# Kernel optimization log

Hardware: AMD Instinct MI355X
Metric: run time of the kernel (lower is better)

## Reference

```python
import jax, jax.numpy as jnp
import numpy as np

N, T, H, E = 16384, 4, 64, 262144
NEG_SLOPE = 0.2  # LeakyReLU slope for GAT-style attention
LN_EPS = 1e-5


def setup_inputs() -> dict:
    key = jax.random.key(0)
    ks = jax.random.split(key, 24)
    p = {}
    p["pred"] = jax.random.normal(ks[0], (N, T, H), jnp.float32)
    p["ei_structural"] = jax.random.randint(ks[1], (2, E), 0, N, jnp.int32)
    p["ei_functional"] = jax.random.randint(ks[2], (2, E), 0, N, jnp.int32)
    scale = 1.0 / np.sqrt(H)
    i = 3
    for l in range(2):
        for et in ("s", "f"):
            p[f"W{l}{et}"] = (jax.random.normal(ks[i], (H, H), jnp.float32) * scale); i += 1
            p[f"a{l}{et}"] = (jax.random.normal(ks[i], (H,), jnp.float32) * scale); i += 1
        p[f"g{l}"] = jnp.ones((H,), jnp.float32)
        p[f"b{l}"] = jnp.zeros((H,), jnp.float32)
    return p


def _conv(x, ei, W, a, n_dst):
    """Attention-based ST graph conv, temporal_kernel_size=1 (per-step)."""
    h = jnp.einsum('nth,hd->ntd', x, W)          # [N,T,H] linear transform
    src, dst = ei[0], ei[1]
    he = h[src]                                   # [E,T,H] gather per edge
    logits = jax.nn.leaky_relu(jnp.einsum('eth,h->et', he, a), NEG_SLOPE)
    m = jax.ops.segment_max(logits, dst, num_segments=n_dst)     # [N,T]
    ex = jnp.exp(logits - m[dst])                 # stable softmax over incoming edges
    den = jax.ops.segment_sum(ex, dst, num_segments=n_dst)
    alpha = ex / den[dst]                         # [E,T]
    return jax.ops.segment_sum(alpha[..., None] * he, dst, num_segments=n_dst)


def _ln(x, g, b):
    mu = x.mean(-1, keepdims=True)
    v = x.var(-1, keepdims=True)
    return (x - mu) * jax.lax.rsqrt(v + LN_EPS) * g + b


def reference(pred, ei_structural, ei_functional,
              W0s, a0s, W0f, a0f, g0, b0,
              W1s, a1s, W1f, a1f, g1, b1):
    x = pred
    layers = ((W0s, a0s, W0f, a0f, g0, b0), (W1s, a1s, W1f, a1f, g1, b1))
    for (Ws, av, Wf, af, g, b) in layers:
        ms = _conv(x, ei_structural, Ws, av, N)
        mf = _conv(x, ei_functional, Wf, af, N)
        # sum(messages)/len(messages), residual, LayerNorm over H (dropout=identity in eval)
        x = _ln(x + 0.5 * (ms + mf), g, b)
    return x
```

## Files before the change

kernel.cpp:

```cpp
#include <hip/hip_runtime.h>
#include <hip/hip_bf16.h>

#define NN 16384
#define TT 4
#define HH 64
#define NT (NN * TT)
#define CAP 128
#define NEG_SLOPE 0.2f
#define LN_EPS 1e-5f

typedef __attribute__((ext_vector_type(8))) short short8;
typedef __attribute__((ext_vector_type(4))) float f32x4;

__device__ __forceinline__ float bf2f(unsigned short u) {
    return __uint_as_float((unsigned)u << 16);
}
__device__ __forceinline__ unsigned short f2bf(float f) {
    unsigned u = __float_as_uint(f);
    return (unsigned short)((u + 0x7FFF + ((u >> 16) & 1)) >> 16);
}


__global__ void zero_kernel(int* __restrict__ a, int n) {
    int i = blockIdx.x * blockDim.x + threadIdx.x;
    if (i < n) a[i] = 0;
}

__global__ void scatter_bucket_kernel(const int* __restrict__ ei_s, const int* __restrict__ ei_f,
                                      int* __restrict__ cnt2, int* __restrict__ col2, int E) {
    int e = blockIdx.x * blockDim.x + threadIdx.x;
    if (e < E) {
        int d = ei_s[E + e];
        int pos = atomicAdd(&cnt2[d], 1);
        if (pos < CAP) col2[d * CAP + pos] = ei_s[e];
    } else {
        e -= E;
        if (e < E) {
            int d = ei_f[E + e];
            int pos = atomicAdd(&cnt2[NN + d], 1);
            if (pos < CAP) col2[(long)NN * CAP + d * CAP + pos] = ei_f[e];
        }
    }
}


__global__ __launch_bounds__(256) void transform2_kernel(
    const float4* __restrict__ x4,
    const float* __restrict__ Ws, const float* __restrict__ as_,
    const float* __restrict__ Wf, const float* __restrict__ af,
    unsigned short* __restrict__ h_s, float* __restrict__ esc_s,
    unsigned short* __restrict__ h_f, float* __restrict__ esc_f) {
    const int lane = threadIdx.x & 63;
    const int wv = threadIdx.x >> 6;
    const int m = lane & 15;
    const int quad = lane >> 4;

    short8 Bs[4][2], Bf[4][2];
#pragma unroll
    for (int c = 0; c < 4; c++) {
#pragma unroll
        for (int ks = 0; ks < 2; ks++) {
#pragma unroll
            for (int j = 0; j < 8; j++) {
                int k = ks * 32 + quad * 8 + j;
                int n = c * 16 + m;
                Bs[c][ks][j] = (short)f2bf(Ws[k * 64 + n]);
                Bf[c][ks][j] = (short)f2bf(Wf[k * 64 + n]);
            }
        }
    }
    float a_s[4], a_f[4];
#pragma unroll
    for (int c = 0; c < 4; c++) { a_s[c] = as_[c * 16 + m]; a_f[c] = af[c * 16 + m]; }

    const int rowbase = blockIdx.x * 128 + wv * 32;
#pragma unroll
    for (int rt = 0; rt < 2; rt++) {
        const int row0 = rowbase + rt * 16;
        const long xbase = (long)(row0 + m) * 16 + quad * 2;
        float4 xa = x4[xbase];
        float4 xb = x4[xbase + 1];
        float4 xc = x4[xbase + 8];
        float4 xd = x4[xbase + 9];
        short8 A0, A1;
        A0[0] = (short)f2bf(xa.x); A0[1] = (short)f2bf(xa.y);
        A0[2] = (short)f2bf(xa.z); A0[3] = (short)f2bf(xa.w);
        A0[4] = (short)f2bf(xb.x); A0[5] = (short)f2bf(xb.y);
        A0[6] = (short)f2bf(xb.z); A0[7] = (short)f2bf(xb.w);
        A1[0] = (short)f2bf(xc.x); A1[1] = (short)f2bf(xc.y);
        A1[2] = (short)f2bf(xc.z); A1[3] = (short)f2bf(xc.w);
        A1[4] = (short)f2bf(xd.x); A1[5] = (short)f2bf(xd.y);
        A1[6] = (short)f2bf(xd.z); A1[7] = (short)f2bf(xd.w);

        f32x4 accs[4], accf[4];
#pragma unroll
        for (int c = 0; c < 4; c++) {
            accs[c] = (f32x4){0.f, 0.f, 0.f, 0.f};
            accf[c] = (f32x4){0.f, 0.f, 0.f, 0.f};
        }
#pragma unroll
        for (int c = 0; c < 4; c++) {
            accs[c] = __builtin_amdgcn_mfma_f32_16x16x32_bf16(A0, Bs[c][0], accs[c], 0, 0, 0);
            accs[c] = __builtin_amdgcn_mfma_f32_16x16x32_bf16(A1, Bs[c][1], accs[c], 0, 0, 0);
            accf[c] = __builtin_amdgcn_mfma_f32_16x16x32_bf16(A0, Bf[c][0], accf[c], 0, 0, 0);
            accf[c] = __builtin_amdgcn_mfma_f32_16x16x32_bf16(A1, Bf[c][1], accf[c], 0, 0, 0);
        }
#pragma unroll
        for (int reg = 0; reg < 4; reg++) {
            const int row = row0 + quad * 4 + reg;
            float ps = 0.f, pf = 0.f;
#pragma unroll
            for (int c = 0; c < 4; c++) {
                h_s[(long)row * 64 + c * 16 + m] = f2bf(accs[c][reg]);
                h_f[(long)row * 64 + c * 16 + m] = f2bf(accf[c][reg]);
                ps = fmaf(accs[c][reg], a_s[c], ps);
                pf = fmaf(accf[c][reg], a_f[c], pf);
            }
#pragma unroll
            for (int off = 1; off < 16; off <<= 1) {
                ps += __shfl_xor(ps, off, 64);
                pf += __shfl_xor(pf, off, 64);
            }
            if (m == 0) {
                float ls = (ps > 0.f) ? ps : NEG_SLOPE * ps;
                float lf = (pf > 0.f) ? pf : NEG_SLOPE * pf;
                esc_s[row] = __expf(ls);
                esc_f[row] = __expf(lf);
            }
        }
    }
}


__global__ __launch_bounds__(256) void aggregate_kernel(
    const float4* __restrict__ x4,
    const ushort4* __restrict__ hs4, const float* __restrict__ escs,
    const int* __restrict__ cnts, const int* __restrict__ cols,
    const ushort4* __restrict__ hf4, const float* __restrict__ escf,
    const int* __restrict__ cntf, const int* __restrict__ colf,
    const float4* __restrict__ g4, const float4* __restrict__ b4,
    float4* __restrict__ out4) {
    const int wv = threadIdx.x >> 6;
    const int lane = threadIdx.x & 63;
    const int n = blockIdx.x * 4 + wv;
    const int t = lane >> 4;
    const int ci = lane & 15;

    int cS = cnts[n]; if (cS > CAP) cS = CAP;
    int cF = cntf[n]; if (cF > CAP) cF = CAP;
    cS = __builtin_amdgcn_readfirstlane(cS);
    cF = __builtin_amdgcn_readfirstlane(cF);
    const int* colS = cols + (long)n * CAP;
    const int* colF = colf + (long)n * CAP;

    int idxS = colS[lane];
    int idxF = colF[lane];
    if (lane >= cS) idxS = 0;
    if (lane >= cF) idxF = 0;

    const int cS64 = cS < 64 ? cS : 64;
    const int cF64 = cF < 64 ? cF : 64;

    float dS = 0.f, sx = 0.f, sy = 0.f, sz = 0.f, sw = 0.f;
    float dF = 0.f, fx = 0.f, fy = 0.f, fz = 0.f, fw = 0.f;

    const int nbS = (cS64 + 7) >> 3;
    const int nbF = (cF64 + 7) >> 3;
    const int nb = nbS > nbF ? nbS : nbF;

    for (int it = 0; it < nb; ++it) {
        const int j = it << 3;
        const bool doS = it < nbS;
        const bool doF = it < nbF;
        int sS[8], sF[8];
        float eS[8], eF[8];
        ushort4 hS[8], hF[8];

        if (doS) {
#pragma unroll
            for (int u = 0; u < 8; u++) sS[u] = __builtin_amdgcn_readlane(idxS, j + u);
#pragma unroll
            for (int u = 0; u < 8; u++) hS[u] = hs4[sS[u] * 64 + lane];
#pragma unroll
            for (int u = 0; u < 8; u++) eS[u] = escs[sS[u] * 4 + t];
        }
        if (doF) {
#pragma unroll
            for (int u = 0; u < 8; u++) sF[u] = __builtin_amdgcn_readlane(idxF, j + u);
#pragma unroll
            for (int u = 0; u < 8; u++) hF[u] = hf4[sF[u] * 64 + lane];
#pragma unroll
            for (int u = 0; u < 8; u++) eF[u] = escf[sF[u] * 4 + t];
        }
        if (doS) {
#pragma unroll
            for (int u = 0; u < 8; u++) {
                float e = (j + u < cS64) ? eS[u] : 0.f;
                dS += e;
                sx = fmaf(e, bf2f(hS[u].x), sx);
                sy = fmaf(e, bf2f(hS[u].y), sy);
                sz = fmaf(e, bf2f(hS[u].z), sz);
                sw = fmaf(e, bf2f(hS[u].w), sw);
            }
        }
        if (doF) {
#pragma unroll
            for (int u = 0; u < 8; u++) {
                float e = (j + u < cF64) ? eF[u] : 0.f;
                dF += e;
                fx = fmaf(e, bf2f(hF[u].x), fx);
                fy = fmaf(e, bf2f(hF[u].y), fy);
                fz = fmaf(e, bf2f(hF[u].z), fz);
                fw = fmaf(e, bf2f(hF[u].w), fw);
            }
        }
    }

    for (int j2 = 64; j2 < cS; ++j2) {
        int s0 = colS[j2];
        float e0 = escs[s0 * 4 + t];
        ushort4 h0 = hs4[(long)s0 * 64 + lane];
        dS += e0;
        sx = fmaf(e0, bf2f(h0.x), sx);
        sy = fmaf(e0, bf2f(h0.y), sy);
        sz = fmaf(e0, bf2f(h0.z), sz);
        sw = fmaf(e0, bf2f(h0.w), sw);
    }
    for (int j2 = 64; j2 < cF; ++j2) {
        int s0 = colF[j2];
        float e0 = escf[s0 * 4 + t];
        ushort4 h0 = hf4[(long)s0 * 64 + lane];
        dF += e0;
        fx = fmaf(e0, bf2f(h0.x), fx);
        fy = fmaf(e0, bf2f(h0.y), fy);
        fz = fmaf(e0, bf2f(h0.z), fz);
        fw = fmaf(e0, bf2f(h0.w), fw);
    }

    float msx = 0.f, msy = 0.f, msz = 0.f, msw = 0.f;
    if (dS > 0.f) {
        float r = 1.f / dS;
        msx = sx * r; msy = sy * r; msz = sz * r; msw = sw * r;
    }
    float mfx = 0.f, mfy = 0.f, mfz = 0.f, mfw = 0.f;
    if (dF > 0.f) {
        float r = 1.f / dF;
        mfx = fx * r; mfy = fy * r; mfz = fz * r; mfw = fw * r;
    }

    float4 xv = x4[(long)n * 64 + lane];
    float v0 = xv.x + 0.5f * (msx + mfx);
    float v1 = xv.y + 0.5f * (msy + mfy);
    float v2 = xv.z + 0.5f * (msz + mfz);
    float v3 = xv.w + 0.5f * (msw + mfw);

    float sum = (v0 + v1) + (v2 + v3);
#pragma unroll
    for (int off = 1; off < 16; off <<= 1) sum += __shfl_xor(sum, off, 64);
    float mu = sum * (1.f / 64.f);
    float d0 = v0 - mu, d1 = v1 - mu, d2 = v2 - mu, d3 = v3 - mu;
    float var = (d0 * d0 + d1 * d1) + (d2 * d2 + d3 * d3);
#pragma unroll
    for (int off = 1; off < 16; off <<= 1) var += __shfl_xor(var, off, 64);
    var *= (1.f / 64.f);
    float inv = rsqrtf(var + LN_EPS);
    float4 gv = g4[ci], bv = b4[ci];
    float4 o;
    o.x = d0 * inv * gv.x + bv.x;
    o.y = d1 * inv * gv.y + bv.y;
    o.z = d2 * inv * gv.z + bv.z;
    o.w = d3 * inv * gv.w + bv.w;
    out4[(long)n * 64 + lane] = o;
}


extern "C" void kernel_launch(void* const* d_in, const int* in_sizes, int n_in,
                              void* d_out, int out_size, void* d_ws, size_t ws_size,
                              hipStream_t stream) {
    const float* pred = (const float*)d_in[0];
    const int* ei_s = (const int*)d_in[1];
    const int* ei_f = (const int*)d_in[2];
    const float* W0s = (const float*)d_in[3];
    const float* a0s = (const float*)d_in[4];
    const float* W0f = (const float*)d_in[5];
    const float* a0f = (const float*)d_in[6];
    const float* g0  = (const float*)d_in[7];
    const float* b0  = (const float*)d_in[8];
    const float* W1s = (const float*)d_in[9];
    const float* a1s = (const float*)d_in[10];
    const float* W1f = (const float*)d_in[11];
    const float* a1f = (const float*)d_in[12];
    const float* g1  = (const float*)d_in[13];
    const float* b1  = (const float*)d_in[14];
    const int E = in_sizes[1] / 2;

    char* ws = (char*)d_ws;
    auto alloc = [&](size_t bytes) {
        char* p = ws;
        ws += (bytes + 255) & ~(size_t)255;
        return p;
    };
    int* cnt2 = (int*)alloc((size_t)2 * NN * sizeof(int));
    int* col2 = (int*)alloc((size_t)2 * NN * CAP * sizeof(int));
    unsigned short* h_s = (unsigned short*)alloc((size_t)NT * HH * sizeof(unsigned short));
    unsigned short* h_f = (unsigned short*)alloc((size_t)NT * HH * sizeof(unsigned short));
    float* esc_s = (float*)alloc((size_t)NT * sizeof(float));
    float* esc_f = (float*)alloc((size_t)NT * sizeof(float));
    float* x_mid = (float*)alloc((size_t)NT * HH * sizeof(float));

    const int* cnt_s = cnt2;
    const int* cnt_f = cnt2 + NN;
    const int* col_s = col2;
    const int* col_f = col2 + (size_t)NN * CAP;

    const int EB = (E + 255) / 256;

    zero_kernel<<<(2 * NN) / 256, 256, 0, stream>>>(cnt2, 2 * NN);
    scatter_bucket_kernel<<<2 * EB, 256, 0, stream>>>(ei_s, ei_f, cnt2, col2, E);

    transform2_kernel<<<NT / 128, 256, 0, stream>>>(
        (const float4*)pred, W0s, a0s, W0f, a0f, h_s, esc_s, h_f, esc_f);
    aggregate_kernel<<<NN / 4, 256, 0, stream>>>(
        (const float4*)pred, (const ushort4*)h_s, esc_s, cnt_s, col_s,
        (const ushort4*)h_f, esc_f, cnt_f, col_f,
        (const float4*)g0, (const float4*)b0, (float4*)x_mid);

    transform2_kernel<<<NT / 128, 256, 0, stream>>>(
        (const float4*)x_mid, W1s, a1s, W1f, a1f, h_s, esc_s, h_f, esc_f);
    aggregate_kernel<<<NN / 4, 256, 0, stream>>>(
        (const float4*)x_mid, (const ushort4*)h_s, esc_s, cnt_s, col_s,
        (const ushort4*)h_f, esc_f, cnt_f, col_f,
        (const float4*)g1, (const float4*)b1, (float4*)d_out);
}
```

Measured before the change: 220.0 us.

## Fuse all stages into persistent mega-kernel with software grid barriers

```diff
diff --git a/kernel.cpp b/kernel.cpp
--- a/kernel.cpp
+++ b/kernel.cpp
@@ -8,6 +8,7 @@
 #define CAP 128
 #define NEG_SLOPE 0.2f
 #define LN_EPS 1e-5f
+#define MEGA_BLOCKS 512
 
 typedef __attribute__((ext_vector_type(8))) short short8;
 typedef __attribute__((ext_vector_type(4))) float f32x4;
@@ -21,21 +22,66 @@
 }
 
 
-__global__ void zero_kernel(int* __restrict__ a, int n) {
-    int i = blockIdx.x * blockDim.x + threadIdx.x;
-    if (i < n) a[i] = 0;
-}
-
-__global__ void scatter_bucket_kernel(const int* __restrict__ ei_s, const int* __restrict__ ei_f,
-                                      int* __restrict__ cnt2, int* __restrict__ col2, int E) {
-    int e = blockIdx.x * blockDim.x + threadIdx.x;
-    if (e < E) {
-        int d = ei_s[E + e];
-        int pos = atomicAdd(&cnt2[d], 1);
-        if (pos < CAP) col2[d * CAP + pos] = ei_s[e];
-    } else {
-        e -= E;
+__device__ __forceinline__ void gridbar(int* bar) {
+    __syncthreads();
+    if (threadIdx.x == 0) {
+        __threadfence();
+        int g = __hip_atomic_load(&bar[1], __ATOMIC_RELAXED, __HIP_MEMORY_SCOPE_AGENT);
+        int a = atomicAdd(&bar[0], 1);
+        if (a == MEGA_BLOCKS - 1) {
+            __hip_atomic_store(&bar[0], 0, __ATOMIC_RELAXED, __HIP_MEMORY_SCOPE_AGENT);
+            __hip_atomic_store(&bar[1], g + 1, __ATOMIC_RELEASE, __HIP_MEMORY_SCOPE_AGENT);
+        } else {
+            while (__hip_atomic_load(&bar[1], __ATOMIC_ACQUIRE, __HIP_MEMORY_SCOPE_AGENT) == g)
+                __builtin_amdgcn_s_sleep(2);
+        }
+        __threadfence();
+    }
+    __syncthreads();
+}
+
+
+__global__ __launch_bounds__(256) void prep_kernel(
+    const float* __restrict__ W0s_, const float* __restrict__ W0f_,
+    const float* __restrict__ W1s_, const float* __restrict__ W1f_,
+    short8* __restrict__ wpack, int* __restrict__ cnt2, int* __restrict__ bar) {
+    const int b = blockIdx.x;
+    if (b < 128) {
+        cnt2[b * 256 + threadIdx.x] = 0;
+        if (b == 0 && threadIdx.x < 2) bar[threadIdx.x] = 0;
+        return;
+    }
+    int id = (b - 128) * 256 + threadIdx.x;
+    int mat = id >> 9;
+    int slot = id & 511;
+    int lane = slot & 63;
+    int cks = slot >> 6;
+    int c = cks >> 1, ks = cks & 1;
+    int m = lane & 15, quad = lane >> 4;
+    const float* W = (mat == 0) ? W0s_ : (mat == 1) ? W0f_ : (mat == 2) ? W1s_ : W1f_;
+    short8 v;
+#pragma unroll
+    for (int j = 0; j < 8; j++) {
+        int k = ks * 32 + quad * 8 + j;
+        int n = c * 16 + m;
+        v[j] = (short)f2bf(W[k * 64 + n]);
+    }
+    wpack[id] = v;
+}
+
+
+__device__ __forceinline__ void scatter_body(const int* __restrict__ ei_s,
+                                             const int* __restrict__ ei_f,
+                                             int* __restrict__ cnt2,
+                                             int* __restrict__ col2, int E) {
+    for (int e0 = blockIdx.x * 256 + threadIdx.x; e0 < 2 * E; e0 += MEGA_BLOCKS * 256) {
+        int e = e0;
         if (e < E) {
+            int d = ei_s[E + e];
+            int pos = atomicAdd(&cnt2[d], 1);
+            if (pos < CAP) col2[d * CAP + pos] = ei_s[e];
+        } else {
+            e -= E;
             int d = ei_f[E + e];
             int pos = atomicAdd(&cnt2[NN + d], 1);
             if (pos < CAP) col2[(long)NN * CAP + d * CAP + pos] = ei_f[e];
@@ -44,10 +90,10 @@
 }
 
 
-__global__ __launch_bounds__(256) void transform2_kernel(
+__device__ __forceinline__ void transform_body(
     const float4* __restrict__ x4,
-    const float* __restrict__ Ws, const float* __restrict__ as_,
-    const float* __restrict__ Wf, const float* __restrict__ af,
+    const short8* __restrict__ wp_s, const float* __restrict__ as_,
+    const short8* __restrict__ wp_f, const float* __restrict__ af,
     unsigned short* __restrict__ h_s, float* __restrict__ esc_s,
     unsigned short* __restrict__ h_f, float* __restrict__ esc_f) {
     const int lane = threadIdx.x & 63;
@@ -60,13 +106,8 @@
     for (int c = 0; c < 4; c++) {
 #pragma unroll
         for (int ks = 0; ks < 2; ks++) {
-#pragma unroll
-            for (int j = 0; j < 8; j++) {
-                int k = ks * 32 + quad * 8 + j;
-                int n = c * 16 + m;
-                Bs[c][ks][j] = (short)f2bf(Ws[k * 64 + n]);
-                Bf[c][ks][j] = (short)f2bf(Wf[k * 64 + n]);
-            }
+            Bs[c][ks] = wp_s[(c * 2 + ks) * 64 + lane];
+            Bf[c][ks] = wp_f[(c * 2 + ks) * 64 + lane];
         }
     }
     float a_s[4], a_f[4];
@@ -132,7 +173,7 @@
 }
 
 
-__global__ __launch_bounds__(256) void aggregate_kernel(
+__device__ __forceinline__ void aggregate_body(
     const float4* __restrict__ x4,
     const ushort4* __restrict__ hs4, const float* __restrict__ escs,
     const int* __restrict__ cnts, const int* __restrict__ cols,
@@ -142,135 +183,172 @@
     float4* __restrict__ out4) {
     const int wv = threadIdx.x >> 6;
     const int lane = threadIdx.x & 63;
-    const int n = blockIdx.x * 4 + wv;
     const int t = lane >> 4;
     const int ci = lane & 15;
-
-    int cS = cnts[n]; if (cS > CAP) cS = CAP;
-    int cF = cntf[n]; if (cF > CAP) cF = CAP;
-    cS = __builtin_amdgcn_readfirstlane(cS);
-    cF = __builtin_amdgcn_readfirstlane(cF);
-    const int* colS = cols + (long)n * CAP;
-    const int* colF = colf + (long)n * CAP;
-
-    int idxS = colS[lane];
-    int idxF = colF[lane];
-    if (lane >= cS) idxS = 0;
-    if (lane >= cF) idxF = 0;
-
-    const int cS64 = cS < 64 ? cS : 64;
-    const int cF64 = cF < 64 ? cF : 64;
-
-    float dS = 0.f, sx = 0.f, sy = 0.f, sz = 0.f, sw = 0.f;
-    float dF = 0.f, fx = 0.f, fy = 0.f, fz = 0.f, fw = 0.f;
-
-    const int nbS = (cS64 + 7) >> 3;
-    const int nbF = (cF64 + 7) >> 3;
-    const int nb = nbS > nbF ? nbS : nbF;
-
-    for (int it = 0; it < nb; ++it) {
-        const int j = it << 3;
-        const bool doS = it < nbS;
-        const bool doF = it < nbF;
-        int sS[8], sF[8];
-        float eS[8], eF[8];
-        ushort4 hS[8], hF[8];
-
-        if (doS) {
-#pragma unroll
-            for (int u = 0; u < 8; u++) sS[u] = __builtin_amdgcn_readlane(idxS, j + u);
-#pragma unroll
-            for (int u = 0; u < 8; u++) hS[u] = hs4[sS[u] * 64 + lane];
-#pragma unroll
-            for (int u = 0; u < 8; u++) eS[u] = escs[sS[u] * 4 + t];
-        }
-        if (doF) {
-#pragma unroll
-            for (int u = 0; u < 8; u++) sF[u] = __builtin_amdgcn_readlane(idxF, j + u);
-#pragma unroll
-            for (int u = 0; u < 8; u++) hF[u] = hf4[sF[u] * 64 + lane];
-#pragma unroll
-            for (int u = 0; u < 8; u++) eF[u] = escf[sF[u] * 4 + t];
-        }
-        if (doS) {
-#pragma unroll
-            for (int u = 0; u < 8; u++) {
-                float e = (j + u < cS64) ? eS[u] : 0.f;
-                dS += e;
-                sx = fmaf(e, bf2f(hS[u].x), sx);
-                sy = fmaf(e, bf2f(hS[u].y), sy);
-                sz = fmaf(e, bf2f(hS[u].z), sz);
-                sw = fmaf(e, bf2f(hS[u].w), sw);
-            }
-        }
-        if (doF) {
-#pragma unroll
-            for (int u = 0; u < 8; u++) {
-                float e = (j + u < cF64) ? eF[u] : 0.f;
-                dF += e;
-                fx = fmaf(e, bf2f(hF[u].x), fx);
-                fy = fmaf(e, bf2f(hF[u].y), fy);
-                fz = fmaf(e, bf2f(hF[u].z), fz);
-                fw = fmaf(e, bf2f(hF[u].w), fw);
-            }
-        }
-    }
-
-    for (int j2 = 64; j2 < cS; ++j2) {
-        int s0 = colS[j2];
-        float e0 = escs[s0 * 4 + t];
-        ushort4 h0 = hs4[(long)s0 * 64 + lane];
-        dS += e0;
-        sx = fmaf(e0, bf2f(h0.x), sx);
-        sy = fmaf(e0, bf2f(h0.y), sy);
-        sz = fmaf(e0, bf2f(h0.z), sz);
-        sw = fmaf(e0, bf2f(h0.w), sw);
-    }
-    for (int j2 = 64; j2 < cF; ++j2) {
-        int s0 = colF[j2];
-        float e0 = escf[s0 * 4 + t];
-        ushort4 h0 = hf4[(long)s0 * 64 + lane];
-        dF += e0;
-        fx = fmaf(e0, bf2f(h0.x), fx);
-        fy = fmaf(e0, bf2f(h0.y), fy);
-        fz = fmaf(e0, bf2f(h0.z), fz);
-        fw = fmaf(e0, bf2f(h0.w), fw);
-    }
-
-    float msx = 0.f, msy = 0.f, msz = 0.f, msw = 0.f;
-    if (dS > 0.f) {
-        float r = 1.f / dS;
-        msx = sx * r; msy = sy * r; msz = sz * r; msw = sw * r;
-    }
-    float mfx = 0.f, mfy = 0.f, mfz = 0.f, mfw = 0.f;
-    if (dF > 0.f) {
-        float r = 1.f / dF;
-        mfx = fx * r; mfy = fy * r; mfz = fz * r; mfw = fw * r;
-    }
-
-    float4 xv = x4[(long)n * 64 + lane];
-    float v0 = xv.x + 0.5f * (msx + mfx);
-    float v1 = xv.y + 0.5f * (msy + mfy);
-    float v2 = xv.z + 0.5f * (msz + mfz);
-    float v3 = xv.w + 0.5f * (msw + mfw);
-
-    float sum = (v0 + v1) + (v2 + v3);
-#pragma unroll
-    for (int off = 1; off < 16; off <<= 1) sum += __shfl_xor(sum, off, 64);
-    float mu = sum * (1.f / 64.f);
-    float d0 = v0 - mu, d1 = v1 - mu, d2 = v2 - mu, d3 = v3 - mu;
-    float var = (d0 * d0 + d1 * d1) + (d2 * d2 + d3 * d3);
-#pragma unroll
-    for (int off = 1; off < 16; off <<= 1) var += __shfl_xor(var, off, 64);
-    var *= (1.f / 64.f);
-    float inv = rsqrtf(var + LN_EPS);
-    float4 gv = g4[ci], bv = b4[ci];
-    float4 o;
-    o.x = d0 * inv * gv.x + bv.x;
-    o.y = d1 * inv * gv.y + bv.y;
-    o.z = d2 * inv * gv.z + bv.z;
-    o.w = d3 * inv * gv.w + bv.w;
-    out4[(long)n * 64 + lane] = o;
+    const float4 gv = g4[ci], bv = b4[ci];
+    const int n0 = (blockIdx.x * 4 + wv) * 8;
+
+    for (int i = 0; i < 8; ++i) {
+        const int n = n0 + i;
+        int cS = cnts[n]; if (cS > CAP) cS = CAP;
+        int cF = cntf[n]; if (cF > CAP) cF = CAP;
+        cS = __builtin_amdgcn_readfirstlane(cS);
+        cF = __builtin_amdgcn_readfirstlane(cF);
+        const int* colS = cols + (long)n * CAP;
+        const int* colF = colf + (long)n * CAP;
+
+        int idxS = colS[lane];
+        int idxF = colF[lane];
+        if (lane >= cS) idxS = 0;
+        if (lane >= cF) idxF = 0;
+
+        const int cS64 = cS < 64 ? cS : 64;
+        const int cF64 = cF < 64 ? cF : 64;
+
+        float dS = 0.f, sx = 0.f, sy = 0.f, sz = 0.f, sw = 0.f;
+        float dF = 0.f, fx = 0.f, fy = 0.f, fz = 0.f, fw = 0.f;
+
+        const int nbS = (cS64 + 7) >> 3;
+        const int nbF = (cF64 + 7) >> 3;
+        const int nb = nbS > nbF ? nbS : nbF;
+
+        for (int it = 0; it < nb; ++it) {
+            const int j = it << 3;
+            const bool doS = it < nbS;
+            const bool doF = it < nbF;
+            int sS[8], sF[8];
+            float eS[8], eF[8];
+            ushort4 hS[8], hF[8];
+
+            if (doS) {
+#pragma unroll
+                for (int u = 0; u < 8; u++) sS[u] = __builtin_amdgcn_readlane(idxS, j + u);
+#pragma unroll
+                for (int u = 0; u < 8; u++) hS[u] = hs4[sS[u] * 64 + lane];
+#pragma unroll
+                for (int u = 0; u < 8; u++) eS[u] = escs[sS[u] * 4 + t];
+            }
+            if (doF) {
+#pragma unroll
+                for (int u = 0; u < 8; u++) sF[u] = __builtin_amdgcn_readlane(idxF, j + u);
+#pragma unroll
+                for (int u = 0; u < 8; u++) hF[u] = hf4[sF[u] * 64 + lane];
+#pragma unroll
+                for (int u = 0; u < 8; u++) eF[u] = escf[sF[u] * 4 + t];
+            }
+            if (doS) {
+#pragma unroll
+                for (int u = 0; u < 8; u++) {
+                    float e = (j + u < cS64) ? eS[u] : 0.f;
+                    dS += e;
+                    sx = fmaf(e, bf2f(hS[u].x), sx);
+                    sy = fmaf(e, bf2f(hS[u].y), sy);
+                    sz = fmaf(e, bf2f(hS[u].z), sz);
+                    sw = fmaf(e, bf2f(hS[u].w), sw);
+                }
+            }
+            if (doF) {
+#pragma unroll
+                for (int u = 0; u < 8; u++) {
+                    float e = (j + u < cF64) ? eF[u] : 0.f;
+                    dF += e;
+                    fx = fmaf(e, bf2f(hF[u].x), fx);
+                    fy = fmaf(e, bf2f(hF[u].y), fy);
+                    fz = fmaf(e, bf2f(hF[u].z), fz);
+                    fw = fmaf(e, bf2f(hF[u].w), fw);
+                }
+            }
+        }
+
+        for (int j2 = 64; j2 < cS; ++j2) {
+            int s0 = colS[j2];
+            float e0 = escs[s0 * 4 + t];
+            ushort4 h0 = hs4[(long)s0 * 64 + lane];
+            dS += e0;
+            sx = fmaf(e0, bf2f(h0.x), sx);
+            sy = fmaf(e0, bf2f(h0.y), sy);
+            sz = fmaf(e0, bf2f(h0.z), sz);
+            sw = fmaf(e0, bf2f(h0.w), sw);
+        }
+        for (int j2 = 64; j2 < cF; ++j2) {
+            int s0 = colF[j2];
+            float e0 = escf[s0 * 4 + t];
+            ushort4 h0 = hf4[(long)s0 * 64 + lane];
+            dF += e0;
+            fx = fmaf(e0, bf2f(h0.x), fx);
+            fy = fmaf(e0, bf2f(h0.y), fy);
+            fz = fmaf(e0, bf2f(h0.z), fz);
+            fw = fmaf(e0, bf2f(h0.w), fw);
+        }
+
+        float msx = 0.f, msy = 0.f, msz = 0.f, msw = 0.f;
+        if (dS > 0.f) {
+            float r = 1.f / dS;
+            msx = sx * r; msy = sy * r; msz = sz * r; msw = sw * r;
+        }
+        float mfx = 0.f, mfy = 0.f, mfz = 0.f, mfw = 0.f;
+        if (dF > 0.f) {
+            float r = 1.f / dF;
+            mfx = fx * r; mfy = fy * r; mfz = fz * r; mfw = fw * r;
+        }
+
+        float4 xv = x4[(long)n * 64 + lane];
+        float v0 = xv.x + 0.5f * (msx + mfx);
+        float v1 = xv.y + 0.5f * (msy + mfy);
+        float v2 = xv.z + 0.5f * (msz + mfz);
+        float v3 = xv.w + 0.5f * (msw + mfw);
+
+        float sum = (v0 + v1) + (v2 + v3);
+#pragma unroll
+        for (int off = 1; off < 16; off <<= 1) sum += __shfl_xor(sum, off, 64);
+        float mu = sum * (1.f / 64.f);
+        float d0 = v0 - mu, d1 = v1 - mu, d2 = v2 - mu, d3 = v3 - mu;
+        float var = (d0 * d0 + d1 * d1) + (d2 * d2 + d3 * d3);
+#pragma unroll
+        for (int off = 1; off < 16; off <<= 1) var += __shfl_xor(var, off, 64);
+        var *= (1.f / 64.f);
+        float inv = rsqrtf(var + LN_EPS);
+        float4 o;
+        o.x = d0 * inv * gv.x + bv.x;
+        o.y = d1 * inv * gv.y + bv.y;
+        o.z = d2 * inv * gv.z + bv.z;
+        o.w = d3 * inv * gv.w + bv.w;
+        out4[(long)n * 64 + lane] = o;
+    }
+}
+
+
+__global__ __launch_bounds__(256, 2) void mega_kernel(
+    const int* __restrict__ ei_s, const int* __restrict__ ei_f, int E,
+    int* __restrict__ cnt2, int* __restrict__ col2,
+    const float4* __restrict__ pred,
+    const short8* __restrict__ wpack,
+    const float* __restrict__ a0s, const float* __restrict__ a0f,
+    const float4* __restrict__ g0, const float4* __restrict__ b0,
+    const float* __restrict__ a1s, const float* __restrict__ a1f,
+    const float4* __restrict__ g1, const float4* __restrict__ b1,
+    unsigned short* __restrict__ h_s, unsigned short* __restrict__ h_f,
+    float* __restrict__ esc_s, float* __restrict__ esc_f,
+    float4* __restrict__ x_mid, float4* __restrict__ out,
+    int* __restrict__ bar) {
+    const int* cnt_s = cnt2;
+    const int* cnt_f = cnt2 + NN;
+    const int* col_s = col2;
+    const int* col_f = col2 + (size_t)NN * CAP;
+
+    scatter_body(ei_s, ei_f, cnt2, col2, E);
+    gridbar(bar);
+
+    transform_body(pred, wpack, a0s, wpack + 512, a0f, h_s, esc_s, h_f, esc_f);
+    gridbar(bar);
+    aggregate_body(pred, (const ushort4*)h_s, esc_s, cnt_s, col_s,
+                   (const ushort4*)h_f, esc_f, cnt_f, col_f, g0, b0, x_mid);
+    gridbar(bar);
+
+    transform_body(x_mid, wpack + 1024, a1s, wpack + 1536, a1f, h_s, esc_s, h_f, esc_f);
+    gridbar(bar);
+    aggregate_body(x_mid, (const ushort4*)h_s, esc_s, cnt_s, col_s,
+                   (const ushort4*)h_f, esc_f, cnt_f, col_f, g1, b1, out);
 }
 
 
@@ -302,33 +380,21 @@
     };
     int* cnt2 = (int*)alloc((size_t)2 * NN * sizeof(int));
     int* col2 = (int*)alloc((size_t)2 * NN * CAP * sizeof(int));
+    short8* wpack = (short8*)alloc((size_t)4 * 512 * sizeof(short8));
     unsigned short* h_s = (unsigned short*)alloc((size_t)NT * HH * sizeof(unsigned short));
     unsigned short* h_f = (unsigned short*)alloc((size_t)NT * HH * sizeof(unsigned short));
     float* esc_s = (float*)alloc((size_t)NT * sizeof(float));
     float* esc_f = (float*)alloc((size_t)NT * sizeof(float));
     float* x_mid = (float*)alloc((size_t)NT * HH * sizeof(float));
-
-    const int* cnt_s = cnt2;
-    const int* cnt_f = cnt2 + NN;
-    const int* col_s = col2;
-    const int* col_f = col2 + (size_t)NN * CAP;
-
-    const int EB = (E + 255) / 256;
-
-    zero_kernel<<<(2 * NN) / 256, 256, 0, stream>>>(cnt2, 2 * NN);
-    scatter_bucket_kernel<<<2 * EB, 256, 0, stream>>>(ei_s, ei_f, cnt2, col2, E);
-
-    transform2_kernel<<<NT / 128, 256, 0, stream>>>(
-        (const float4*)pred, W0s, a0s, W0f, a0f, h_s, esc_s, h_f, esc_f);
-    aggregate_kernel<<<NN / 4, 256, 0, stream>>>(
-        (const float4*)pred, (const ushort4*)h_s, esc_s, cnt_s, col_s,
-        (const ushort4*)h_f, esc_f, cnt_f, col_f,
-        (const float4*)g0, (const float4*)b0, (float4*)x_mid);
-
-    transform2_kernel<<<NT / 128, 256, 0, stream>>>(
-        (const float4*)x_mid, W1s, a1s, W1f, a1f, h_s, esc_s, h_f, esc_f);
-    aggregate_kernel<<<NN / 4, 256, 0, stream>>>(
-        (const float4*)x_mid, (const ushort4*)h_s, esc_s, cnt_s, col_s,
-        (const ushort4*)h_f, esc_f, cnt_f, col_f,
-        (const float4*)g1, (const float4*)b1, (float4*)d_out);
-}
+    int* bar = (int*)alloc(2 * sizeof(int));
+
+    prep_kernel<<<136, 256, 0, stream>>>(W0s, W0f, W1s, W1f, wpack, cnt2, bar);
+
+    mega_kernel<<<MEGA_BLOCKS, 256, 0, stream>>>(
+        ei_s, ei_f, E, cnt2, col2,
+        (const float4*)pred, wpack,
+        a0s, a0f, (const float4*)g0, (const float4*)b0,
+        a1s, a1f, (const float4*)g1, (const float4*)b1,
+        h_s, h_f, esc_s, esc_f,
+        (float4*)x_mid, (float4*)d_out, bar);
+}
```

Measured after the change: 596.7 us. +171.3%, slower.
